# Performance work log

Hardware: AMD Instinct MI355X
Metric: run time of the kernel (lower is better)

Reference implementation:

```python
import jax, jax.numpy as jnp
import numpy as np


def setup_inputs() -> dict:
    key = jax.random.key(0)
    k = jax.random.split(key, 6)
    B = 65536
    return {
        "x": jax.random.normal(k[0], (B, 784), dtype=jnp.float32),
        "conv_w": jax.random.normal(k[1], (3, 3), dtype=jnp.float32),
        "fc1_w": jax.random.normal(k[2], (128, 676), dtype=jnp.float32) * 0.04,
        "fc1_b": jax.random.normal(k[3], (128,), dtype=jnp.float32),
        "fc2_w": jax.random.normal(k[4], (10, 128), dtype=jnp.float32) * 0.09,
        "fc2_b": jax.random.normal(k[5], (10,), dtype=jnp.float32),
    }


def reference(x, conv_w, fc1_w, fc1_b, fc2_w, fc2_b):
    B = x.shape[0]
    img = x.reshape(B, 1, 28, 28)  # NCHW, single channel
    # Valid cross-correlation with a 3x3 kernel (matches the torch sum(region*weight) loop)
    kern = conv_w.reshape(1, 1, 3, 3)  # OIHW
    conv = jax.lax.conv_general_dilated(
        img, kern, window_strides=(1, 1), padding="VALID",
        dimension_numbers=("NCHW", "OIHW", "NCHW"))  # [B,1,26,26]
    h = conv.reshape(B, 26 * 26)
    h = jax.nn.relu(h @ fc1_w.T + fc1_b)  # [B,128]
    logits = h @ fc2_w.T + fc2_b  # [B,10]
    return logits
```

## Files before the change

kernel.cpp:

```cpp
#include <hip/hip_runtime.h>

typedef __bf16 bf16x8 __attribute__((ext_vector_type(8)));
typedef float  f32x4  __attribute__((ext_vector_type(4)));

#define KDIM    784
#define KSTEP   32
#define NSTEPS  25
#define NCOLS   128
#define NT      8
#define WAVES   4
#define ROWS_PER_WAVE 32
#define ROWS_PER_BLOCK (WAVES * ROWS_PER_WAVE)
#define STAGE_BYTES 16384
#define HSH_PAD 132
#define HCHUNK  16

__global__ __launch_bounds__(256) void prep_weff(
    const float* __restrict__ conv_w,
    const float* __restrict__ fc1_w,
    __bf16* __restrict__ wfrag)
{
  int idx = blockIdx.x * 256 + threadIdx.x;
  if (idx >= NSTEPS * NT * 64) return;
  int lane = idx & 63;
  int n    = (idx >> 6) & (NT - 1);
  int s    = idx >> 9;
  int col  = n * 16 + (lane & 15);
  int kb   = s * KSTEP + (lane >> 4) * 8;
  bf16x8 o;
#pragma unroll
  for (int j = 0; j < 8; ++j) {
    int k = kb + j;
    float v = 0.f;
    if (k < KDIM) {
      int r = k / 28, c = k % 28;
#pragma unroll
      for (int u = 0; u < 3; ++u)
#pragma unroll
        for (int w = 0; w < 3; ++w) {
          int p = r - u, q = c - w;
          if (p >= 0 && p < 26 && q >= 0 && q < 26)
            v = fmaf(conv_w[u * 3 + w], fc1_w[col * 676 + p * 26 + q], v);
        }
    }
    o[j] = (__bf16)v;
  }
  reinterpret_cast<bf16x8*>(wfrag)[idx] = o;
}

__device__ __forceinline__ bf16x8 pack8(f32x4 lo, f32x4 hi) {
  bf16x8 r;
  r[0] = (__bf16)lo[0]; r[1] = (__bf16)lo[1];
  r[2] = (__bf16)lo[2]; r[3] = (__bf16)lo[3];
  r[4] = (__bf16)hi[0]; r[5] = (__bf16)hi[1];
  r[6] = (__bf16)hi[2]; r[7] = (__bf16)hi[3];
  return r;
}

__device__ __forceinline__ void split8(f32x4 a, f32x4 b, bf16x8& hi, bf16x8& lo) {
#pragma unroll
  for (int j = 0; j < 4; ++j) {
    __bf16 h = (__bf16)a[j]; hi[j] = h; lo[j] = (__bf16)(a[j] - (float)h);
  }
#pragma unroll
  for (int j = 0; j < 4; ++j) {
    __bf16 h = (__bf16)b[j]; hi[4 + j] = h; lo[4 + j] = (__bf16)(b[j] - (float)h);
  }
}

__device__ __forceinline__ void stage_issue(
    const __bf16* __restrict__ wfrag, unsigned char* dstbuf,
    int stage, int wave, int lane, int nchunks)
{
#pragma unroll
  for (int c = 0; c < 4; ++c) {
    int cw = wave * 4 + c;
    if (cw < nchunks) {
      const unsigned char* src =
          (const unsigned char*)wfrag + (size_t)stage * STAGE_BYTES + cw * 1024 + lane * 16;
      unsigned char* dst = dstbuf + cw * 1024 + lane * 16;
      __builtin_amdgcn_global_load_lds(
          (const __attribute__((address_space(1))) unsigned int*)src,
          (__attribute__((address_space(3))) unsigned int*)dst,
          16, 0, 0);
    }
  }
}

__global__ __launch_bounds__(256, 3) void fused_mlp(
    const float*  __restrict__ x,
    const __bf16* __restrict__ wfrag,
    const float*  __restrict__ fc1_b,
    const float*  __restrict__ fc2_w,
    const float*  __restrict__ fc2_b,
    float*        __restrict__ out)
{
  __shared__ __align__(16) unsigned char smem[WAVES * HCHUNK * HSH_PAD * 4];
  float (*hsh)[HCHUNK][HSH_PAD] =
      reinterpret_cast<float (*)[HCHUNK][HSH_PAD]>(smem);

  int tid  = threadIdx.x;
  int wave = tid >> 6, lane = tid & 63;
  int lrow = lane & 15;
  int lgrp = lane >> 4;
  long wrow0 = (long)blockIdx.x * ROWS_PER_BLOCK + wave * ROWS_PER_WAVE;

  const float* xr0 = x + (wrow0 + lrow) * KDIM;
  const float* xr1 = xr0 + 16 * KDIM;

  f32x4 acc[2][NT];
#pragma unroll
  for (int m = 0; m < 2; ++m)
#pragma unroll
    for (int n = 0; n < NT; ++n) acc[m][n] = (f32x4){0.f, 0.f, 0.f, 0.f};

  f32x4 xv[8];
#define LOAD_STAGE(T)                                          \
  {                                                            \
    int k0 = (2 * (T)) * KSTEP + lgrp * 8;                     \
    xv[0] = *(const f32x4*)(xr0 + k0);                         \
    xv[1] = *(const f32x4*)(xr0 + k0 + 4);                     \
    xv[2] = *(const f32x4*)(xr1 + k0);                         \
    xv[3] = *(const f32x4*)(xr1 + k0 + 4);                     \
    xv[4] = *(const f32x4*)(xr0 + k0 + KSTEP);                 \
    xv[5] = *(const f32x4*)(xr0 + k0 + KSTEP + 4);             \
    xv[6] = *(const f32x4*)(xr1 + k0 + KSTEP);                 \
    xv[7] = *(const f32x4*)(xr1 + k0 + KSTEP + 4);             \
  }

  stage_issue(wfrag, smem, 0, wave, lane, 16);
  LOAD_STAGE(0);
  int cur = 0;

  for (int t = 0; t < 12; ++t) {
    __syncthreads();
    stage_issue(wfrag, smem + (cur ^ 1) * STAGE_BYTES, t + 1, wave, lane,
                (t < 11) ? 16 : 8);

    bf16x8 a00 = pack8(xv[0], xv[1]), a01 = pack8(xv[2], xv[3]);
    bf16x8 a10 = pack8(xv[4], xv[5]), a11 = pack8(xv[6], xv[7]);

    if (t < 11) {
      LOAD_STAGE(t + 1);
    } else {
      if (lgrp < 2) {
        int k = (NSTEPS - 1) * KSTEP + lgrp * 8;
        xv[0] = *(const f32x4*)(xr0 + k);
        xv[1] = *(const f32x4*)(xr0 + k + 4);
        xv[2] = *(const f32x4*)(xr1 + k);
        xv[3] = *(const f32x4*)(xr1 + k + 4);
      } else {
        xv[0] = (f32x4){0.f,0.f,0.f,0.f}; xv[1] = (f32x4){0.f,0.f,0.f,0.f};
        xv[2] = (f32x4){0.f,0.f,0.f,0.f}; xv[3] = (f32x4){0.f,0.f,0.f,0.f};
      }
    }

    const bf16x8* bp = (const bf16x8*)(smem + cur * STAGE_BYTES) + lane;
    {
      bf16x8 bf[NT];
#pragma unroll
      for (int n = 0; n < NT; ++n) bf[n] = bp[n * 64];
#pragma unroll
      for (int n = 0; n < NT; ++n) {
        acc[0][n] = __builtin_amdgcn_mfma_f32_16x16x32_bf16(a00, bf[n], acc[0][n], 0, 0, 0);
        acc[1][n] = __builtin_amdgcn_mfma_f32_16x16x32_bf16(a01, bf[n], acc[1][n], 0, 0, 0);
      }
    }
    {
      bf16x8 bf[NT];
#pragma unroll
      for (int n = 0; n < NT; ++n) bf[n] = bp[512 + n * 64];
#pragma unroll
      for (int n = 0; n < NT; ++n) {
        acc[0][n] = __builtin_amdgcn_mfma_f32_16x16x32_bf16(a10, bf[n], acc[0][n], 0, 0, 0);
        acc[1][n] = __builtin_amdgcn_mfma_f32_16x16x32_bf16(a11, bf[n], acc[1][n], 0, 0, 0);
      }
    }
    cur ^= 1;
  }

  __syncthreads();
  {
    bf16x8 a0 = pack8(xv[0], xv[1]);
    bf16x8 a1 = pack8(xv[2], xv[3]);
    const bf16x8* bp = (const bf16x8*)(smem + cur * STAGE_BYTES) + lane;
#pragma unroll
    for (int n = 0; n < NT; ++n) {
      bf16x8 b = bp[n * 64];
      acc[0][n] = __builtin_amdgcn_mfma_f32_16x16x32_bf16(a0, b, acc[0][n], 0, 0, 0);
      acc[1][n] = __builtin_amdgcn_mfma_f32_16x16x32_bf16(a1, b, acc[1][n], 0, 0, 0);
    }
  }
  __syncthreads();

  int osafe = (lrow < 10) ? lrow : 9;
  bf16x8 whi[4], wlo[4];
#pragma unroll
  for (int s2 = 0; s2 < 4; ++s2) {
    f32x4 w0 = *(const f32x4*)(fc2_w + osafe * NCOLS + s2 * 32 + lgrp * 8);
    f32x4 w1 = *(const f32x4*)(fc2_w + osafe * NCOLS + s2 * 32 + lgrp * 8 + 4);
    if (lrow >= 10) { w0 = (f32x4){0.f,0.f,0.f,0.f}; w1 = (f32x4){0.f,0.f,0.f,0.f}; }
    split8(w0, w1, whi[s2], wlo[s2]);
  }
  float b2 = (lrow < 10) ? fc2_b[lrow] : 0.f;
  float bcol[NT];
#pragma unroll
  for (int n = 0; n < NT; ++n) bcol[n] = fc1_b[n * 16 + lrow];

#pragma unroll
  for (int m2 = 0; m2 < 2; ++m2) {
#pragma unroll
    for (int n = 0; n < NT; ++n) {
      int col = n * 16 + lrow;
#pragma unroll
      for (int ri = 0; ri < 4; ++ri) {
        int rl = lgrp * 4 + ri;
        hsh[wave][rl][col] = fmaxf(acc[m2][n][ri] + bcol[n], 0.f);
      }
    }
    f32x4 acc2 = (f32x4){0.f, 0.f, 0.f, 0.f};
    const float* hr = &hsh[wave][lrow][0];
#pragma unroll
    for (int s2 = 0; s2 < 4; ++s2) {
      f32x4 h0 = *(const f32x4*)(hr + s2 * 32 + lgrp * 8);
      f32x4 h1 = *(const f32x4*)(hr + s2 * 32 + lgrp * 8 + 4);
      bf16x8 ahi, alo; split8(h0, h1, ahi, alo);
      acc2 = __builtin_amdgcn_mfma_f32_16x16x32_bf16(ahi, whi[s2], acc2, 0, 0, 0);
      acc2 = __builtin_amdgcn_mfma_f32_16x16x32_bf16(ahi, wlo[s2], acc2, 0, 0, 0);
      acc2 = __builtin_amdgcn_mfma_f32_16x16x32_bf16(alo, whi[s2], acc2, 0, 0, 0);
    }
    if (lrow < 10) {
#pragma unroll
      for (int ri = 0; ri < 4; ++ri)
        out[(wrow0 + m2 * 16 + lgrp * 4 + ri) * 10 + lrow] = acc2[ri] + b2;
    }
  }
}

extern "C" void kernel_launch(void* const* d_in, const int* in_sizes, int n_in,
                              void* d_out, int out_size, void* d_ws, size_t ws_size,
                              hipStream_t stream) {
  const float* x      = (const float*)d_in[0];
  const float* conv_w = (const float*)d_in[1];
  const float* fc1_w  = (const float*)d_in[2];
  const float* fc1_b  = (const float*)d_in[3];
  const float* fc2_w  = (const float*)d_in[4];
  const float* fc2_b  = (const float*)d_in[5];
  float* outp = (float*)d_out;
  __bf16* wfrag = (__bf16*)d_ws;

  int Btotal = in_sizes[0] / KDIM;
  int prep_threads = NSTEPS * NT * 64;

  hipLaunchKernelGGL(prep_weff, dim3((prep_threads + 255) / 256), dim3(256), 0, stream,
                     conv_w, fc1_w, wfrag);
  hipLaunchKernelGGL(fused_mlp, dim3(Btotal / ROWS_PER_BLOCK), dim3(256), 0, stream,
                     x, wfrag, fc1_b, fc2_w, fc2_b, outp);
}
```

Baseline: 50.86 us.

## Double-buffer x registers with explicit vmcnt waits and unrolled K loop

Splits the activation registers into current and next sets so the next x tile's global loads are issued before the MFMA work on the current tile. Replaces __syncthreads with an explicit s_waitcnt vmcnt(8) plus s_barrier under sched_barrier fences, so only the LDS weight stage must land before proceeding while the x loads stay in flight. The loop is fully unrolled with a peeled final step, and launch bounds drop from 3 to 2 blocks per SIMD to leave room for the extra registers. This risks lower occupancy, and the hand-counted vmcnt assumes a particular issue order.

```diff
diff --git a/kernel.cpp b/kernel.cpp
--- a/kernel.cpp
+++ b/kernel.cpp
@@ -87,7 +87,7 @@
   }
 }
 
-__global__ __launch_bounds__(256, 3) void fused_mlp(
+__global__ __launch_bounds__(256, 2) void fused_mlp(
     const float*  __restrict__ x,
     const __bf16* __restrict__ wfrag,
     const float*  __restrict__ fc1_b,
@@ -114,46 +114,39 @@
 #pragma unroll
     for (int n = 0; n < NT; ++n) acc[m][n] = (f32x4){0.f, 0.f, 0.f, 0.f};
 
-  f32x4 xv[8];
-#define LOAD_STAGE(T)                                          \
+  f32x4 xc[8], xn[8];
+#define LOAD_X(T, V)                                           \
   {                                                            \
     int k0 = (2 * (T)) * KSTEP + lgrp * 8;                     \
-    xv[0] = *(const f32x4*)(xr0 + k0);                         \
-    xv[1] = *(const f32x4*)(xr0 + k0 + 4);                     \
-    xv[2] = *(const f32x4*)(xr1 + k0);                         \
-    xv[3] = *(const f32x4*)(xr1 + k0 + 4);                     \
-    xv[4] = *(const f32x4*)(xr0 + k0 + KSTEP);                 \
-    xv[5] = *(const f32x4*)(xr0 + k0 + KSTEP + 4);             \
-    xv[6] = *(const f32x4*)(xr1 + k0 + KSTEP);                 \
-    xv[7] = *(const f32x4*)(xr1 + k0 + KSTEP + 4);             \
+    V[0] = *(const f32x4*)(xr0 + k0);                          \
+    V[1] = *(const f32x4*)(xr0 + k0 + 4);                      \
+    V[2] = *(const f32x4*)(xr1 + k0);                          \
+    V[3] = *(const f32x4*)(xr1 + k0 + 4);                      \
+    V[4] = *(const f32x4*)(xr0 + k0 + KSTEP);                  \
+    V[5] = *(const f32x4*)(xr0 + k0 + KSTEP + 4);              \
+    V[6] = *(const f32x4*)(xr1 + k0 + KSTEP);                  \
+    V[7] = *(const f32x4*)(xr1 + k0 + KSTEP + 4);              \
   }
 
   stage_issue(wfrag, smem, 0, wave, lane, 16);
-  LOAD_STAGE(0);
+  __builtin_amdgcn_sched_barrier(0);
+  LOAD_X(0, xc);
+  __builtin_amdgcn_sched_barrier(0);
+  asm volatile("s_waitcnt vmcnt(8)" ::: "memory");
+  __builtin_amdgcn_sched_barrier(0);
+  __builtin_amdgcn_s_barrier();
+  __builtin_amdgcn_sched_barrier(0);
+
   int cur = 0;
-
-  for (int t = 0; t < 12; ++t) {
-    __syncthreads();
-    stage_issue(wfrag, smem + (cur ^ 1) * STAGE_BYTES, t + 1, wave, lane,
-                (t < 11) ? 16 : 8);
-
-    bf16x8 a00 = pack8(xv[0], xv[1]), a01 = pack8(xv[2], xv[3]);
-    bf16x8 a10 = pack8(xv[4], xv[5]), a11 = pack8(xv[6], xv[7]);
-
-    if (t < 11) {
-      LOAD_STAGE(t + 1);
-    } else {
-      if (lgrp < 2) {
-        int k = (NSTEPS - 1) * KSTEP + lgrp * 8;
-        xv[0] = *(const f32x4*)(xr0 + k);
-        xv[1] = *(const f32x4*)(xr0 + k + 4);
-        xv[2] = *(const f32x4*)(xr1 + k);
-        xv[3] = *(const f32x4*)(xr1 + k + 4);
-      } else {
-        xv[0] = (f32x4){0.f,0.f,0.f,0.f}; xv[1] = (f32x4){0.f,0.f,0.f,0.f};
-        xv[2] = (f32x4){0.f,0.f,0.f,0.f}; xv[3] = (f32x4){0.f,0.f,0.f,0.f};
-      }
-    }
+#pragma unroll
+  for (int t = 0; t < 11; ++t) {
+    stage_issue(wfrag, smem + (cur ^ 1) * STAGE_BYTES, t + 1, wave, lane, 16);
+    __builtin_amdgcn_sched_barrier(0);
+    LOAD_X(t + 1, xn);
+    __builtin_amdgcn_sched_barrier(0);
+
+    bf16x8 a00 = pack8(xc[0], xc[1]), a01 = pack8(xc[2], xc[3]);
+    bf16x8 a10 = pack8(xc[4], xc[5]), a11 = pack8(xc[6], xc[7]);
 
     const bf16x8* bp = (const bf16x8*)(smem + cur * STAGE_BYTES) + lane;
     {
@@ -176,13 +169,61 @@
         acc[1][n] = __builtin_amdgcn_mfma_f32_16x16x32_bf16(a11, bf[n], acc[1][n], 0, 0, 0);
       }
     }
+    __builtin_amdgcn_sched_barrier(0);
+    asm volatile("s_waitcnt vmcnt(8)" ::: "memory");
+    __builtin_amdgcn_sched_barrier(0);
+    __builtin_amdgcn_s_barrier();
+    __builtin_amdgcn_sched_barrier(0);
+
+#pragma unroll
+    for (int i = 0; i < 8; ++i) xc[i] = xn[i];
     cur ^= 1;
   }
 
-  __syncthreads();
   {
-    bf16x8 a0 = pack8(xv[0], xv[1]);
-    bf16x8 a1 = pack8(xv[2], xv[3]);
+    stage_issue(wfrag, smem + (cur ^ 1) * STAGE_BYTES, 12, wave, lane, 8);
+    __builtin_amdgcn_sched_barrier(0);
+    if (lgrp < 2) {
+      int k = (NSTEPS - 1) * KSTEP + lgrp * 8;
+      xn[0] = *(const f32x4*)(xr0 + k);
+      xn[1] = *(const f32x4*)(xr0 + k + 4);
+      xn[2] = *(const f32x4*)(xr1 + k);
+      xn[3] = *(const f32x4*)(xr1 + k + 4);
+    } else {
+      xn[0] = (f32x4){0.f,0.f,0.f,0.f}; xn[1] = (f32x4){0.f,0.f,0.f,0.f};
+      xn[2] = (f32x4){0.f,0.f,0.f,0.f}; xn[3] = (f32x4){0.f,0.f,0.f,0.f};
+    }
+
+    bf16x8 a00 = pack8(xc[0], xc[1]), a01 = pack8(xc[2], xc[3]);
+    bf16x8 a10 = pack8(xc[4], xc[5]), a11 = pack8(xc[6], xc[7]);
+    const bf16x8* bp = (const bf16x8*)(smem + cur * STAGE_BYTES) + lane;
+    {
+      bf16x8 bf[NT];
+#pragma unroll
+      for (int n = 0; n < NT; ++n) bf[n] = bp[n * 64];
+#pragma unroll
+      for (int n = 0; n < NT; ++n) {
+        acc[0][n] = __builtin_amdgcn_mfma_f32_16x16x32_bf16(a00, bf[n], acc[0][n], 0, 0, 0);
+        acc[1][n] = __builtin_amdgcn_mfma_f32_16x16x32_bf16(a01, bf[n], acc[1][n], 0, 0, 0);
+      }
+    }
+    {
+      bf16x8 bf[NT];
+#pragma unroll
+      for (int n = 0; n < NT; ++n) bf[n] = bp[512 + n * 64];
+#pragma unroll
+      for (int n = 0; n < NT; ++n) {
+        acc[0][n] = __builtin_amdgcn_mfma_f32_16x16x32_bf16(a10, bf[n], acc[0][n], 0, 0, 0);
+        acc[1][n] = __builtin_amdgcn_mfma_f32_16x16x32_bf16(a11, bf[n], acc[1][n], 0, 0, 0);
+      }
+    }
+    __syncthreads();
+    cur ^= 1;
+  }
+
+  {
+    bf16x8 a0 = pack8(xn[0], xn[1]);
+    bf16x8 a1 = pack8(xn[2], xn[3]);
     const bf16x8* bp = (const bf16x8*)(smem + cur * STAGE_BYTES) + lane;
 #pragma unroll
     for (int n = 0; n < NT; ++n) {
```

Measured after the change: 52.58 us. 1.03x slower.

## Double stage size to four K-steps with two-register-set x prefetch

Applied to the files above, without the earlier changes.

Each pipeline stage now covers four K-steps (32KB of weight fragments) instead of two, which halves the number of barrier-separated iterations. Two register sets of x activations alternate so the loads for the next half-stage are in flight while MFMAs run on the current one. LDS grows to 64KB per block and launch bounds drop from 3 to 2 blocks per CU, which lowers occupancy and raises register pressure.

```diff
diff --git a/kernel.cpp b/kernel.cpp
--- a/kernel.cpp
+++ b/kernel.cpp
@@ -11,7 +11,9 @@
 #define WAVES   4
 #define ROWS_PER_WAVE 32
 #define ROWS_PER_BLOCK (WAVES * ROWS_PER_WAVE)
-#define STAGE_BYTES 16384
+#define KSTEP_BYTES 8192
+#define STAGE_BYTES 32768
+#define NFULL   6
 #define HSH_PAD 132
 #define HCHUNK  16
 
@@ -69,15 +71,15 @@
 }
 
 __device__ __forceinline__ void stage_issue(
-    const __bf16* __restrict__ wfrag, unsigned char* dstbuf,
-    int stage, int wave, int lane, int nchunks)
+    const __bf16* __restrict__ wfrag, size_t src_off, unsigned char* dstbuf,
+    int wave, int lane, int cpw)
 {
 #pragma unroll
-  for (int c = 0; c < 4; ++c) {
-    int cw = wave * 4 + c;
-    if (cw < nchunks) {
+  for (int c = 0; c < 8; ++c) {
+    if (c < cpw) {
+      int cw = wave * cpw + c;
       const unsigned char* src =
-          (const unsigned char*)wfrag + (size_t)stage * STAGE_BYTES + cw * 1024 + lane * 16;
+          (const unsigned char*)wfrag + src_off + cw * 1024 + lane * 16;
       unsigned char* dst = dstbuf + cw * 1024 + lane * 16;
       __builtin_amdgcn_global_load_lds(
           (const __attribute__((address_space(1))) unsigned int*)src,
@@ -87,7 +89,7 @@
   }
 }
 
-__global__ __launch_bounds__(256, 3) void fused_mlp(
+__global__ __launch_bounds__(256, 2) void fused_mlp(
     const float*  __restrict__ x,
     const __bf16* __restrict__ wfrag,
     const float*  __restrict__ fc1_b,
@@ -95,7 +97,7 @@
     const float*  __restrict__ fc2_b,
     float*        __restrict__ out)
 {
-  __shared__ __align__(16) unsigned char smem[WAVES * HCHUNK * HSH_PAD * 4];
+  __shared__ __align__(16) unsigned char smem[2 * STAGE_BYTES];
   float (*hsh)[HCHUNK][HSH_PAD] =
       reinterpret_cast<float (*)[HCHUNK][HSH_PAD]>(smem);
 
@@ -114,75 +116,90 @@
 #pragma unroll
     for (int n = 0; n < NT; ++n) acc[m][n] = (f32x4){0.f, 0.f, 0.f, 0.f};
 
-  f32x4 xv[8];
-#define LOAD_STAGE(T)                                          \
+  f32x4 xvA[8], xvB[8];
+#define LOAD_X2(E, V)                                          \
   {                                                            \
-    int k0 = (2 * (T)) * KSTEP + lgrp * 8;                     \
-    xv[0] = *(const f32x4*)(xr0 + k0);                         \
-    xv[1] = *(const f32x4*)(xr0 + k0 + 4);                     \
-    xv[2] = *(const f32x4*)(xr1 + k0);                         \
-    xv[3] = *(const f32x4*)(xr1 + k0 + 4);                     \
-    xv[4] = *(const f32x4*)(xr0 + k0 + KSTEP);                 \
-    xv[5] = *(const f32x4*)(xr0 + k0 + KSTEP + 4);             \
-    xv[6] = *(const f32x4*)(xr1 + k0 + KSTEP);                 \
-    xv[7] = *(const f32x4*)(xr1 + k0 + KSTEP + 4);             \
-  }
-
-  stage_issue(wfrag, smem, 0, wave, lane, 16);
-  LOAD_STAGE(0);
+    int k0 = (E) * KSTEP + lgrp * 8;                           \
+    V[0] = *(const f32x4*)(xr0 + k0);                          \
+    V[1] = *(const f32x4*)(xr0 + k0 + 4);                      \
+    V[2] = *(const f32x4*)(xr1 + k0);                          \
+    V[3] = *(const f32x4*)(xr1 + k0 + 4);                      \
+    V[4] = *(const f32x4*)(xr0 + k0 + KSTEP);                  \
+    V[5] = *(const f32x4*)(xr0 + k0 + KSTEP + 4);              \
+    V[6] = *(const f32x4*)(xr1 + k0 + KSTEP);                  \
+    V[7] = *(const f32x4*)(xr1 + k0 + KSTEP + 4);              \
+  }
+
+#define MFMA_GROUP(BASE, O0, O1, V)                                            \
+  {                                                                            \
+    bf16x8 a00 = pack8(V[0], V[1]), a01 = pack8(V[2], V[3]);                   \
+    bf16x8 a10 = pack8(V[4], V[5]), a11 = pack8(V[6], V[7]);                   \
+    const bf16x8* bp0 = (const bf16x8*)((BASE) + (O0)) + lane;                 \
+    {                                                                          \
+      bf16x8 bf[NT];                                                           \
+      _Pragma("unroll")                                                        \
+      for (int n = 0; n < NT; ++n) bf[n] = bp0[n * 64];                        \
+      _Pragma("unroll")                                                        \
+      for (int n = 0; n < NT; ++n) {                                           \
+        acc[0][n] = __builtin_amdgcn_mfma_f32_16x16x32_bf16(a00, bf[n], acc[0][n], 0, 0, 0); \
+        acc[1][n] = __builtin_amdgcn_mfma_f32_16x16x32_bf16(a01, bf[n], acc[1][n], 0, 0, 0); \
+      }                                                                        \
+    }                                                                          \
+    const bf16x8* bp1 = (const bf16x8*)((BASE) + (O1)) + lane;                 \
+    {                                                                          \
+      bf16x8 bf[NT];                                                           \
+      _Pragma("unroll")                                                        \
+      for (int n = 0; n < NT; ++n) bf[n] = bp1[n * 64];                        \
+      _Pragma("unroll")                                                        \
+      for (int n = 0; n < NT; ++n) {                                           \
+        acc[0][n] = __builtin_amdgcn_mfma_f32_16x16x32_bf16(a10, bf[n], acc[0][n], 0, 0, 0); \
+        acc[1][n] = __builtin_amdgcn_mfma_f32_16x16x32_bf16(a11, bf[n], acc[1][n], 0, 0, 0); \
+      }                                                                        \
+    }                                                                          \
+  }
+
+  stage_issue(wfrag, 0, smem, wave, lane, 8);
+  LOAD_X2(0, xvA);
   int cur = 0;
 
-  for (int t = 0; t < 12; ++t) {
+  for (int t = 0; t < NFULL; ++t) {
     __syncthreads();
-    stage_issue(wfrag, smem + (cur ^ 1) * STAGE_BYTES, t + 1, wave, lane,
-                (t < 11) ? 16 : 8);
-
-    bf16x8 a00 = pack8(xv[0], xv[1]), a01 = pack8(xv[2], xv[3]);
-    bf16x8 a10 = pack8(xv[4], xv[5]), a11 = pack8(xv[6], xv[7]);
-
-    if (t < 11) {
-      LOAD_STAGE(t + 1);
+
+    if (t < NFULL - 1)
+      stage_issue(wfrag, (size_t)(t + 1) * STAGE_BYTES,
+                  smem + (cur ^ 1) * STAGE_BYTES, wave, lane, 8);
+    else
+      stage_issue(wfrag, (size_t)24 * KSTEP_BYTES,
+                  smem + (cur ^ 1) * STAGE_BYTES, wave, lane, 2);
+
+    LOAD_X2(4 * t + 2, xvB);
+
+    unsigned char* base = smem + cur * STAGE_BYTES;
+    MFMA_GROUP(base, 0 * KSTEP_BYTES, 1 * KSTEP_BYTES, xvA);
+
+    if (t < NFULL - 1) {
+      LOAD_X2(4 * t + 4, xvA);
     } else {
       if (lgrp < 2) {
-        int k = (NSTEPS - 1) * KSTEP + lgrp * 8;
-        xv[0] = *(const f32x4*)(xr0 + k);
-        xv[1] = *(const f32x4*)(xr0 + k + 4);
-        xv[2] = *(const f32x4*)(xr1 + k);
-        xv[3] = *(const f32x4*)(xr1 + k + 4);
+        int k = 24 * KSTEP + lgrp * 8;
+        xvA[0] = *(const f32x4*)(xr0 + k);
+        xvA[1] = *(const f32x4*)(xr0 + k + 4);
+        xvA[2] = *(const f32x4*)(xr1 + k);
+        xvA[3] = *(const f32x4*)(xr1 + k + 4);
       } else {
-        xv[0] = (f32x4){0.f,0.f,0.f,0.f}; xv[1] = (f32x4){0.f,0.f,0.f,0.f};
-        xv[2] = (f32x4){0.f,0.f,0.f,0.f}; xv[3] = (f32x4){0.f,0.f,0.f,0.f};
+        xvA[0] = (f32x4){0.f,0.f,0.f,0.f}; xvA[1] = (f32x4){0.f,0.f,0.f,0.f};
+        xvA[2] = (f32x4){0.f,0.f,0.f,0.f}; xvA[3] = (f32x4){0.f,0.f,0.f,0.f};
       }
     }
 
-    const bf16x8* bp = (const bf16x8*)(smem + cur * STAGE_BYTES) + lane;
-    {
-      bf16x8 bf[NT];
-#pragma unroll
-      for (int n = 0; n < NT; ++n) bf[n] = bp[n * 64];
-#pragma unroll
-      for (int n = 0; n < NT; ++n) {
-        acc[0][n] = __builtin_amdgcn_mfma_f32_16x16x32_bf16(a00, bf[n], acc[0][n], 0, 0, 0);
-        acc[1][n] = __builtin_amdgcn_mfma_f32_16x16x32_bf16(a01, bf[n], acc[1][n], 0, 0, 0);
-      }
-    }
-    {
-      bf16x8 bf[NT];
-#pragma unroll
-      for (int n = 0; n < NT; ++n) bf[n] = bp[512 + n * 64];
-#pragma unroll
-      for (int n = 0; n < NT; ++n) {
-        acc[0][n] = __builtin_amdgcn_mfma_f32_16x16x32_bf16(a10, bf[n], acc[0][n], 0, 0, 0);
-        acc[1][n] = __builtin_amdgcn_mfma_f32_16x16x32_bf16(a11, bf[n], acc[1][n], 0, 0, 0);
-      }
-    }
+    MFMA_GROUP(base, 2 * KSTEP_BYTES, 3 * KSTEP_BYTES, xvB);
     cur ^= 1;
   }
 
   __syncthreads();
   {
-    bf16x8 a0 = pack8(xv[0], xv[1]);
-    bf16x8 a1 = pack8(xv[2], xv[3]);
+    bf16x8 a0 = pack8(xvA[0], xvA[1]);
+    bf16x8 a1 = pack8(xvA[2], xvA[3]);
     const bf16x8* bp = (const bf16x8*)(smem + cur * STAGE_BYTES) + lane;
 #pragma unroll
     for (int n = 0; n < NT; ++n) {
```

Result: no change. 51.76 us (+1.8%).
